# Kernel tuning notes

Measured on AMD Instinct MI355X. Metric: run time of the kernel, lower is better.

Reference implementation:

```python
import jax, jax.numpy as jnp
import numpy as np

D = 768
EXPAND = 4
D_INNER = EXPAND * D
G = 32
EPS = 1e-5


def setup_inputs() -> dict:
    key = jax.random.key(0)
    ks = jax.random.split(key, 10)
    B, T = 16, G * G
    s = lambda fan_in: 1.0 / np.sqrt(fan_in)
    return {
        "x": jax.random.normal(ks[0], (B, T, D), dtype=jnp.float32),
        "norm_w": jnp.ones((D,), dtype=jnp.float32),
        "w_proj": jax.random.normal(ks[1], (D_INNER, D), dtype=jnp.float32) * s(D),
        "w_gate": jax.random.normal(ks[2], (D_INNER, D), dtype=jnp.float32) * s(D),
        "conv_w": jax.random.normal(ks[3], (D_INNER, 1, 3, 3), dtype=jnp.float32) * s(9),
        "conv_b": jax.random.normal(ks[4], (D_INNER,), dtype=jnp.float32) * 0.01,
        "w_out": jax.random.normal(ks[5], (D, D_INNER), dtype=jnp.float32) * s(D_INNER),
        "w_k": jax.random.normal(ks[6], (D, D), dtype=jnp.float32) * s(D),
        "w_v": jax.random.normal(ks[7], (D, D), dtype=jnp.float32) * s(D),
        "log_alpha": jnp.array(0.0, dtype=jnp.float32),  # log(memory_alpha=1.0)
    }


def _rmsnorm(x, w):
    ms = jnp.mean(jnp.square(x.astype(jnp.float32)), axis=-1, keepdims=True)
    return x * jax.lax.rsqrt(ms + EPS).astype(x.dtype) * w


def reference(x, norm_w, w_proj, w_gate, conv_w, conv_b, w_out, w_k, w_v, log_alpha):
    B, T, _ = x.shape
    h = _rmsnorm(x, norm_w)                                   # [B,T,D]
    val = jnp.einsum("btd,ed->bte", h, w_proj)                # [B,T,dI]
    val = val.transpose(0, 2, 1).reshape(B, D_INNER, G, G)    # [B,dI,G,G]
    val = jax.lax.conv_general_dilated(
        val, conv_w, window_strides=(1, 1), padding=((1, 1), (1, 1)),
        dimension_numbers=("NCHW", "OIHW", "NCHW"),
        feature_group_count=D_INNER,
    ) + conv_b[None, :, None, None]
    val = jax.nn.silu(val)
    val = val.reshape(B, D_INNER, T).transpose(0, 2, 1)       # [B,T,dI]
    gated = val * jax.nn.silu(jnp.einsum("btd,ed->bte", h, w_gate))
    out = jnp.einsum("bte,de->btd", gated, w_out)             # [B,T,D]
    K = jnp.einsum("btd,ed->bte", h, w_k)                     # [B,T,D]
    V = jnp.einsum("btd,ed->bte", out, w_v)                   # [B,T,D]
    W = jnp.einsum("btd,bte->bde", K, V) / T                  # [B,D,D]
    read = jnp.einsum("btd,bde->bte", K, W)                   # [B,T,D]
    out = out + jnp.exp(log_alpha) * read
    return x + out
```

## Files before the change

kernel.cpp:

```cpp
#include <hip/hip_runtime.h>
#include <hip/hip_bf16.h>
#include <cstdint>
#include <cstddef>

typedef unsigned short u16;
typedef __attribute__((ext_vector_type(8))) __bf16 bf16x8;
typedef __attribute__((ext_vector_type(4))) float f32x4;
typedef __attribute__((ext_vector_type(8))) unsigned short us8;

#define NDM 768
#define NDI 3072
#define NTT 1024
#define NBB 16
#define NM (NBB*NTT)

__device__ __forceinline__ u16 f2bf(float f) {
  unsigned u = __builtin_bit_cast(unsigned, f);
  u += 0x7fffu + ((u >> 16) & 1u);
  return (u16)(u >> 16);
}
__device__ __forceinline__ float bf2f(u16 b) {
  return __builtin_bit_cast(float, ((unsigned)b) << 16);
}
__device__ __forceinline__ float silu_f(float v) {
  return v * (1.0f / (1.0f + __expf(-v)));
}
__device__ __forceinline__ void gload16(const u16* g, u16* l) {
  __builtin_amdgcn_global_load_lds((const __attribute__((address_space(1))) void*)g,
                                   (__attribute__((address_space(3))) void*)l, 16, 0, 0);
}

__global__ __launch_bounds__(256)
void k_f32_to_bf16(const float* __restrict__ in, u16* __restrict__ out, int n4) {
  const int i = blockIdx.x * 256 + threadIdx.x;
  if (i < n4) {
    float4 v = ((const float4*)in)[i];
    ushort4 o;
    o.x = f2bf(v.x); o.y = f2bf(v.y); o.z = f2bf(v.z); o.w = f2bf(v.w);
    ((ushort4*)out)[i] = o;
  }
}

__global__ __launch_bounds__(256)
void k_convw_t(const float* __restrict__ cw, u16* __restrict__ wTb) {
  const int e = blockIdx.x * 256 + threadIdx.x;
  if (e < NDI) {
#pragma unroll
    for (int t = 0; t < 9; t++) wTb[t * NDI + e] = f2bf(cw[e * 9 + t]);
  }
}

__global__ __launch_bounds__(256)
void k_rmsnorm(const float* __restrict__ x, const float* __restrict__ w, u16* __restrict__ h) {
  const int row  = blockIdx.x * 4 + (threadIdx.x >> 6);
  const int lane = threadIdx.x & 63;
  const float4* xr = (const float4*)(x + (size_t)row * NDM);
  float4 a = xr[lane], b = xr[lane + 64], c = xr[lane + 128];
  float ss = a.x*a.x + a.y*a.y + a.z*a.z + a.w*a.w
           + b.x*b.x + b.y*b.y + b.z*b.z + b.w*b.w
           + c.x*c.x + c.y*c.y + c.z*c.z + c.w*c.w;
#pragma unroll
  for (int off = 32; off > 0; off >>= 1) ss += __shfl_xor(ss, off);
  const float r = rsqrtf(ss * (1.0f / NDM) + 1e-5f);
  const float4* wr = (const float4*)w;
  float4 wa = wr[lane], wb = wr[lane + 64], wc = wr[lane + 128];
  ushort4 oa, ob, oc;
  oa.x = f2bf(a.x * r * wa.x); oa.y = f2bf(a.y * r * wa.y);
  oa.z = f2bf(a.z * r * wa.z); oa.w = f2bf(a.w * r * wa.w);
  ob.x = f2bf(b.x * r * wb.x); ob.y = f2bf(b.y * r * wb.y);
  ob.z = f2bf(b.z * r * wb.z); ob.w = f2bf(b.w * r * wb.w);
  oc.x = f2bf(c.x * r * wc.x); oc.y = f2bf(c.y * r * wc.y);
  oc.z = f2bf(c.z * r * wc.z); oc.w = f2bf(c.w * r * wc.w);
  ushort4* hr = (ushort4*)(h + (size_t)row * NDM);
  hr[lane] = oa; hr[lane + 64] = ob; hr[lane + 128] = oc;
}

__device__ __forceinline__ void stage8k(const u16* Asrc, const u16* Bsrc, u16* smem,
                                        int cur, int wid, int Kd) {
  u16* Ad = smem + cur * 16384 + wid * 512;
  u16* Bd = smem + 32768 + cur * 16384 + wid * 512;
  const size_t blk = (size_t)64 * Kd;
#pragma unroll
  for (int i = 0; i < 4; i++) {
    gload16(Asrc + i * blk, Ad + i * 4096);
    gload16(Bsrc + i * blk, Bd + i * 4096);
  }
}

template <int MODE>
__global__ __launch_bounds__(512, 2)
void k_g8(const u16* __restrict__ A, const u16* __restrict__ B,
          void* __restrict__ C0, void* __restrict__ C1,
          const float* __restrict__ X, const float* __restrict__ scalep,
          int N, int Kd, int nkt, int nTiles,
          long sAb, long sBb, long sCb, int mPerBatchB, long sBm) {
  __shared__ u16 smem[65536];
  const int bz = blockIdx.z;
  A += (size_t)bz * sAb;
  B += (size_t)bz * sBb;
  const int nwg = gridDim.x;
  const int id = blockIdx.x;
  const int sid = ((nwg & 7) == 0) ? ((id & 7) * (nwg >> 3) + (id >> 3)) : id;
  const int mt = sid / nTiles, ntile = sid - mt * nTiles;
  const int m0 = mt * 256, n0 = ntile * 256;
  if (mPerBatchB > 0) B += (size_t)(m0 / mPerBatchB) * sBm;

  const int tid = threadIdx.x;
  const int lane = tid & 63, wid = tid >> 6;
  const int wm = wid >> 2, wn = wid & 3;
  const int fr = lane & 15, l4 = lane >> 4;

  const int srow = tid >> 3;
  const int sslot = (tid & 7) ^ (srow & 7);
  const u16* Asrc = A + (size_t)(m0 + srow) * Kd + sslot * 8;
  const u16* Bsrc = B + (size_t)(n0 + srow) * Kd + sslot * 8;

  f32x4 acc[8][4];
#pragma unroll
  for (int m = 0; m < 8; m++)
#pragma unroll
    for (int n = 0; n < 4; n++) acc[m][n] = (f32x4){0.f, 0.f, 0.f, 0.f};

  stage8k(Asrc,      Bsrc,      smem, 0, wid, Kd);
  stage8k(Asrc + 64, Bsrc + 64, smem, 1, wid, Kd);

  int cur = 0;
#pragma unroll 1
  for (int t = 0; t < nkt; t++) {
    if (t == nkt - 1) asm volatile("s_waitcnt vmcnt(0)" ::: "memory");
    else              asm volatile("s_waitcnt vmcnt(8)" ::: "memory");
    __builtin_amdgcn_s_barrier();

    const u16* Abuf = smem + cur * 16384;
    const u16* Bbuf = smem + 32768 + cur * 16384;

    bf16x8 bfrag[4][2];
#pragma unroll
    for (int nf = 0; nf < 4; nf++) {
      const int brow = wn * 64 + nf * 16 + fr;
#pragma unroll
      for (int s = 0; s < 2; s++)
        bfrag[nf][s] = *(const bf16x8*)&Bbuf[brow * 64 + (((s << 2) + l4) ^ (brow & 7)) * 8];
    }
#pragma unroll
    for (int mf = 0; mf < 8; mf++) {
      const int arow = wm * 128 + mf * 16 + fr;
      bf16x8 a0 = *(const bf16x8*)&Abuf[arow * 64 + ((l4)     ^ (arow & 7)) * 8];
      bf16x8 a1 = *(const bf16x8*)&Abuf[arow * 64 + ((4 + l4) ^ (arow & 7)) * 8];
#pragma unroll
      for (int nf = 0; nf < 4; nf++) {
        acc[mf][nf] = __builtin_amdgcn_mfma_f32_16x16x32_bf16(a0, bfrag[nf][0], acc[mf][nf], 0, 0, 0);
        acc[mf][nf] = __builtin_amdgcn_mfma_f32_16x16x32_bf16(a1, bfrag[nf][1], acc[mf][nf], 0, 0, 0);
      }
    }
    asm volatile("s_waitcnt lgkmcnt(0)" ::: "memory");
    __builtin_amdgcn_s_barrier();
    if (t < nkt - 2) stage8k(Asrc + (size_t)(t + 2) * 64, Bsrc + (size_t)(t + 2) * 64,
                             smem, cur, wid, Kd);
    cur ^= 1;
  }

  float sc = 1.0f;
  if (MODE == 2) sc = __expf(scalep[0]) * (1.0f / 1024.0f);
  const size_t cb = (size_t)bz * sCb;
#pragma unroll
  for (int mf = 0; mf < 8; mf++) {
#pragma unroll
    for (int nf = 0; nf < 4; nf++) {
      const int lc = wn * 64 + nf * 16 + fr;
      const int rb = m0 + wm * 128 + mf * 16 + (l4 << 2);
#pragma unroll
      for (int q = 0; q < 4; q++) {
        float v = acc[mf][nf][q];
        if (MODE == 0) {
          ((u16*)C0)[cb + (size_t)(rb + q) * N + n0 + lc] = f2bf(v);
        } else if (MODE == 2) {
          ((u16*)C0)[cb + (size_t)(rb + q) * N + n0 + lc] = f2bf(v * sc);
        } else if (MODE == 3) {
          const size_t idx = (size_t)(rb + q) * N + n0 + lc;
          ((float*)C0)[idx] = X[idx] + bf2f(((const u16*)C1)[idx]) + v;
        } else {
          const int gc = n0 + lc;
          if (gc < 3072) ((u16*)C0)[(size_t)(rb + q) * 3072 + gc] = f2bf(v);
          else           ((u16*)C1)[(size_t)(rb + q) * 3072 + gc - 3072] = f2bf(silu_f(v));
        }
      }
    }
  }
}

__global__ __launch_bounds__(384)
void k_conv_gate(const u16* __restrict__ val, u16* __restrict__ gate,
                 const u16* __restrict__ wTb, const float* __restrict__ bias) {
  const int tid = threadIdx.x;
  const int m = blockIdx.x * 2 + (tid >= 192);
  const int e0 = (tid % 192) * 16;
  const int j = m & 31, i = (m >> 5) & 31;
  float acc[16];
  {
    const float4* bp = (const float4*)(bias + e0);
    float4 b0 = bp[0], b1 = bp[1], b2 = bp[2], b3 = bp[3];
    acc[0]=b0.x; acc[1]=b0.y; acc[2]=b0.z; acc[3]=b0.w;
    acc[4]=b1.x; acc[5]=b1.y; acc[6]=b1.z; acc[7]=b1.w;
    acc[8]=b2.x; acc[9]=b2.y; acc[10]=b2.z; acc[11]=b2.w;
    acc[12]=b3.x; acc[13]=b3.y; acc[14]=b3.z; acc[15]=b3.w;
  }
  const u16* vb = val + (size_t)m * NDI + e0;
#pragma unroll
  for (int di = -1; di <= 1; di++) {
    if ((unsigned)(i + di) >= 32u) continue;
#pragma unroll
    for (int dj = -1; dj <= 1; dj++) {
      if ((unsigned)(j + dj) >= 32u) continue;
      const u16* vp = vb + (ptrdiff_t)(di * 32 + dj) * NDI;
      us8 v0 = *(const us8*)vp, v1 = *(const us8*)(vp + 8);
      const u16* wp = wTb + ((di + 1) * 3 + (dj + 1)) * NDI + e0;
      us8 w0 = *(const us8*)wp, w1 = *(const us8*)(wp + 8);
#pragma unroll
      for (int q = 0; q < 8; q++) acc[q]     += bf2f(v0[q]) * bf2f(w0[q]);
#pragma unroll
      for (int q = 0; q < 8; q++) acc[8 + q] += bf2f(v1[q]) * bf2f(w1[q]);
    }
  }
  u16* gp = gate + (size_t)m * NDI + e0;
  us8 g0 = *(const us8*)gp, g1 = *(const us8*)(gp + 8);
  us8 o0, o1;
#pragma unroll
  for (int q = 0; q < 8; q++) o0[q] = f2bf(silu_f(acc[q]) * bf2f(g0[q]));
#pragma unroll
  for (int q = 0; q < 8; q++) o1[q] = f2bf(silu_f(acc[8 + q]) * bf2f(g1[q]));
  *(us8*)gp = o0;
  *(us8*)(gp + 8) = o1;
}

__global__ __launch_bounds__(256)
void k_transpose(const u16* __restrict__ in, u16* __restrict__ out) {
  __shared__ u16 tile[64][65];
  const int d0 = blockIdx.x * 64, t0 = blockIdx.y * 64, b = blockIdx.z;
  const int lx = threadIdx.x & 15, ly = threadIdx.x >> 4;
  const u16* ip = in + ((size_t)b * NTT + t0) * NDM + d0;
#pragma unroll
  for (int p = 0; p < 4; p++) {
    const int r = ly + p * 16;
    ushort4 v = *(const ushort4*)(ip + (size_t)r * NDM + lx * 4);
    tile[r][lx * 4 + 0] = v.x; tile[r][lx * 4 + 1] = v.y;
    tile[r][lx * 4 + 2] = v.z; tile[r][lx * 4 + 3] = v.w;
  }
  __syncthreads();
  u16* op = out + ((size_t)b * NDM + d0) * NTT + t0;
#pragma unroll
  for (int p = 0; p < 4; p++) {
    const int r = ly + p * 16;
    ushort4 v;
    v.x = tile[lx * 4 + 0][r]; v.y = tile[lx * 4 + 1][r];
    v.z = tile[lx * 4 + 2][r]; v.w = tile[lx * 4 + 3][r];
    *(ushort4*)(op + (size_t)r * NTT + lx * 4) = v;
  }
}

extern "C" void kernel_launch(void* const* d_in, const int* in_sizes, int n_in,
                              void* d_out, int out_size, void* d_ws, size_t ws_size,
                              hipStream_t stream) {
  const float* x      = (const float*)d_in[0];
  const float* norm_w = (const float*)d_in[1];
  const float* w_proj = (const float*)d_in[2];
  const float* w_gate = (const float*)d_in[3];
  const float* conv_w = (const float*)d_in[4];
  const float* conv_b = (const float*)d_in[5];
  const float* w_out  = (const float*)d_in[6];
  const float* w_k    = (const float*)d_in[7];
  const float* w_v    = (const float*)d_in[8];
  const float* lalpha = (const float*)d_in[9];

  char* ob = (char*)d_out;
  u16* h    = (u16*)(ob);
  u16* wcat = (u16*)(ob + 25165824);
  u16* wob  = (u16*)(ob + 34603008);
  u16* wkb  = (u16*)(ob + 39321600);
  u16* wvb  = (u16*)(ob + 40501248);
  u16* wTb  = (u16*)(ob + 41680896);

  char* ws = (char*)d_ws;
  u16* valp  = (u16*)(ws);
  u16* gateb = (u16*)(ws + 100663296);
  u16* outb  = (u16*)(ws);
  u16* Kbf   = (u16*)(ws + 25165824);
  u16* Vbf   = (u16*)(ws + 50331648);
  u16* Kt    = (u16*)(ws + 100663296);
  u16* Vt    = (u16*)(ws + 125829120);
  u16* Wt    = (u16*)(ws + 150994944);

  k_f32_to_bf16<<<2304, 256, 0, stream>>>(w_proj, wcat,           589824);
  k_f32_to_bf16<<<2304, 256, 0, stream>>>(w_gate, wcat + 2359296, 589824);
  k_f32_to_bf16<<<2304, 256, 0, stream>>>(w_out,  wob, 589824);
  k_f32_to_bf16<<<576,  256, 0, stream>>>(w_k,    wkb, 147456);
  k_f32_to_bf16<<<576,  256, 0, stream>>>(w_v,    wvb, 147456);
  k_convw_t<<<12, 256, 0, stream>>>(conv_w, wTb);

  k_rmsnorm<<<4096, 256, 0, stream>>>(x, norm_w, h);

  k_g8<5><<<1536, 512, 0, stream>>>(h, wcat, valp, gateb, nullptr, nullptr,
                                    3072, 768, 12, 24, 0, 0, 0, 0, 0);
  k_conv_gate<<<8192, 384, 0, stream>>>(valp, gateb, wTb, conv_b);

  k_g8<0><<<192, 512, 0, stream>>>(gateb, wob, outb, nullptr, nullptr, nullptr,
                                   768, 3072, 48, 3, 0, 0, 0, 0, 0);
  k_g8<0><<<192, 512, 0, stream>>>(h, wkb, Kbf, nullptr, nullptr, nullptr,
                                   768, 768, 12, 3, 0, 0, 0, 0, 0);
  k_g8<0><<<192, 512, 0, stream>>>(outb, wvb, Vbf, nullptr, nullptr, nullptr,
                                   768, 768, 12, 3, 0, 0, 0, 0, 0);
  k_transpose<<<dim3(12, 16, 16), 256, 0, stream>>>(Kbf, Kt);
  k_transpose<<<dim3(12, 16, 16), 256, 0, stream>>>(Vbf, Vt);

  k_g8<2><<<dim3(9, 1, 16), 512, 0, stream>>>(Vt, Kt, Wt, nullptr, nullptr, lalpha,
                                              768, 1024, 16, 3,
                                              (long)NDM * NTT, (long)NDM * NTT,
                                              (long)NDM * NDM, 0, 0);
  k_g8<3><<<192, 512, 0, stream>>>(Kbf, Wt, d_out, outb, x, nullptr,
                                   768, 768, 12, 3, 0, 0, 0,
                                   NTT, (long)NDM * NDM);
}
```

Measured before the change: 701.3 us.

## Switch GEMM mainloop to 4-buffer, 32-wide K stages with deeper prefetch

The bf16 MFMA GEMM now moves through K in 32-element stages across four LDS buffers instead of 64-element stages across two. Loads run three stages ahead, which removes the second barrier per iteration. Each stage reads all fragments before issuing the next prefetch, then runs the MFMAs at raised wave priority. In exchange there are twice as many loop iterations and barriers, and the LDS swizzle becomes a 4-slot XOR pattern that may cause more bank conflicts.

Result: no change. 703.3 us (+0.3%).

```diff
diff --git a/kernel.cpp b/kernel.cpp
--- a/kernel.cpp
+++ b/kernel.cpp
@@ -75,24 +75,12 @@
   hr[lane] = oa; hr[lane + 64] = ob; hr[lane + 128] = oc;
 }
 
-__device__ __forceinline__ void stage8k(const u16* Asrc, const u16* Bsrc, u16* smem,
-                                        int cur, int wid, int Kd) {
-  u16* Ad = smem + cur * 16384 + wid * 512;
-  u16* Bd = smem + 32768 + cur * 16384 + wid * 512;
-  const size_t blk = (size_t)64 * Kd;
-#pragma unroll
-  for (int i = 0; i < 4; i++) {
-    gload16(Asrc + i * blk, Ad + i * 4096);
-    gload16(Bsrc + i * blk, Bd + i * 4096);
-  }
-}
-
 template <int MODE>
 __global__ __launch_bounds__(512, 2)
 void k_g8(const u16* __restrict__ A, const u16* __restrict__ B,
           void* __restrict__ C0, void* __restrict__ C1,
           const float* __restrict__ X, const float* __restrict__ scalep,
-          int N, int Kd, int nkt, int nTiles,
+          int N, int Kd, int nst, int nTiles,
           long sAb, long sBb, long sCb, int mPerBatchB, long sBm) {
   __shared__ u16 smem[65536];
   const int bz = blockIdx.z;
@@ -110,10 +98,21 @@
   const int wm = wid >> 2, wn = wid & 3;
   const int fr = lane & 15, l4 = lane >> 4;
 
-  const int srow = tid >> 3;
-  const int sslot = (tid & 7) ^ (srow & 7);
-  const u16* Asrc = A + (size_t)(m0 + srow) * Kd + sslot * 8;
-  const u16* Bsrc = B + (size_t)(n0 + srow) * Kd + sslot * 8;
+  const int rbase = (wid << 4) + (lane >> 2);
+  const int cslot = (lane & 3) ^ ((lane >> 2) & 3);
+  const u16* Ap = A + (size_t)(m0 + rbase) * Kd + cslot * 8;
+  const u16* Bp = B + (size_t)(n0 + rbase) * Kd + cslot * 8;
+  const size_t strideI = (size_t)128 * Kd;
+  const int ldsW = wid * 512;
+
+#define STAGE_G8(s_) {                                         \
+    const int b3_ = (s_) & 3;                                  \
+    const u16* as_ = Ap + (size_t)(s_) * 32;                   \
+    const u16* bs_ = Bp + (size_t)(s_) * 32;                   \
+    u16* ad_ = smem + b3_ * 8192 + ldsW;                       \
+    u16* bd_ = smem + 32768 + b3_ * 8192 + ldsW;               \
+    gload16(as_, ad_);           gload16(as_ + strideI, ad_ + 4096); \
+    gload16(bs_, bd_);           gload16(bs_ + strideI, bd_ + 4096); }
 
   f32x4 acc[8][4];
 #pragma unroll
@@ -121,44 +120,45 @@
 #pragma unroll
     for (int n = 0; n < 4; n++) acc[m][n] = (f32x4){0.f, 0.f, 0.f, 0.f};
 
-  stage8k(Asrc,      Bsrc,      smem, 0, wid, Kd);
-  stage8k(Asrc + 64, Bsrc + 64, smem, 1, wid, Kd);
-
-  int cur = 0;
+  STAGE_G8(0); STAGE_G8(1); STAGE_G8(2);
+
 #pragma unroll 1
-  for (int t = 0; t < nkt; t++) {
-    if (t == nkt - 1) asm volatile("s_waitcnt vmcnt(0)" ::: "memory");
-    else              asm volatile("s_waitcnt vmcnt(8)" ::: "memory");
+  for (int s = 0; s < nst; s++) {
+    const int left = nst - 1 - s;
+    if (left >= 2)      asm volatile("s_waitcnt vmcnt(8)" ::: "memory");
+    else if (left == 1) asm volatile("s_waitcnt vmcnt(4)" ::: "memory");
+    else                asm volatile("s_waitcnt vmcnt(0)" ::: "memory");
     __builtin_amdgcn_s_barrier();
-
-    const u16* Abuf = smem + cur * 16384;
-    const u16* Bbuf = smem + 32768 + cur * 16384;
-
-    bf16x8 bfrag[4][2];
+    __builtin_amdgcn_sched_barrier(0);
+
+    const int b = s & 3;
+    const u16* Ab = smem + b * 8192;
+    const u16* Bb = smem + 32768 + b * 8192;
+
+    bf16x8 bfr[4];
 #pragma unroll
     for (int nf = 0; nf < 4; nf++) {
       const int brow = wn * 64 + nf * 16 + fr;
-#pragma unroll
-      for (int s = 0; s < 2; s++)
-        bfrag[nf][s] = *(const bf16x8*)&Bbuf[brow * 64 + (((s << 2) + l4) ^ (brow & 7)) * 8];
+      bfr[nf] = *(const bf16x8*)&Bb[brow * 32 + ((l4 ^ (brow & 3)) << 3)];
     }
+    bf16x8 af[8];
 #pragma unroll
     for (int mf = 0; mf < 8; mf++) {
       const int arow = wm * 128 + mf * 16 + fr;
-      bf16x8 a0 = *(const bf16x8*)&Abuf[arow * 64 + ((l4)     ^ (arow & 7)) * 8];
-      bf16x8 a1 = *(const bf16x8*)&Abuf[arow * 64 + ((4 + l4) ^ (arow & 7)) * 8];
-#pragma unroll
-      for (int nf = 0; nf < 4; nf++) {
-        acc[mf][nf] = __builtin_amdgcn_mfma_f32_16x16x32_bf16(a0, bfrag[nf][0], acc[mf][nf], 0, 0, 0);
-        acc[mf][nf] = __builtin_amdgcn_mfma_f32_16x16x32_bf16(a1, bfrag[nf][1], acc[mf][nf], 0, 0, 0);
-      }
+      af[mf] = *(const bf16x8*)&Ab[arow * 32 + ((l4 ^ (arow & 3)) << 3)];
     }
-    asm volatile("s_waitcnt lgkmcnt(0)" ::: "memory");
-    __builtin_amdgcn_s_barrier();
-    if (t < nkt - 2) stage8k(Asrc + (size_t)(t + 2) * 64, Bsrc + (size_t)(t + 2) * 64,
-                             smem, cur, wid, Kd);
-    cur ^= 1;
-  }
+
+    if (s + 3 < nst) STAGE_G8(s + 3);
+
+    __builtin_amdgcn_s_setprio(1);
+#pragma unroll
+    for (int mf = 0; mf < 8; mf++)
+#pragma unroll
+      for (int nf = 0; nf < 4; nf++)
+        acc[mf][nf] = __builtin_amdgcn_mfma_f32_16x16x32_bf16(af[mf], bfr[nf], acc[mf][nf], 0, 0, 0);
+    __builtin_amdgcn_s_setprio(0);
+  }
+#undef STAGE_G8
 
   float sc = 1.0f;
   if (MODE == 2) sc = __expf(scalep[0]) * (1.0f / 1024.0f);
@@ -300,23 +300,23 @@
   k_rmsnorm<<<4096, 256, 0, stream>>>(x, norm_w, h);
 
   k_g8<5><<<1536, 512, 0, stream>>>(h, wcat, valp, gateb, nullptr, nullptr,
-                                    3072, 768, 12, 24, 0, 0, 0, 0, 0);
+                                    3072, 768, 24, 24, 0, 0, 0, 0, 0);
   k_conv_gate<<<8192, 384, 0, stream>>>(valp, gateb, wTb, conv_b);
 
   k_g8<0><<<192, 512, 0, stream>>>(gateb, wob, outb, nullptr, nullptr, nullptr,
-                                   768, 3072, 48, 3, 0, 0, 0, 0, 0);
+                                   768, 3072, 96, 3, 0, 0, 0, 0, 0);
   k_g8<0><<<192, 512, 0, stream>>>(h, wkb, Kbf, nullptr, nullptr, nullptr,
-                                   768, 768, 12, 3, 0, 0, 0, 0, 0);
+                                   768, 768, 24, 3, 0, 0, 0, 0, 0);
   k_g8<0><<<192, 512, 0, stream>>>(outb, wvb, Vbf, nullptr, nullptr, nullptr,
-                                   768, 768, 12, 3, 0, 0, 0, 0, 0);
+                                   768, 768, 24, 3, 0, 0, 0, 0, 0);
   k_transpose<<<dim3(12, 16, 16), 256, 0, stream>>>(Kbf, Kt);
   k_transpose<<<dim3(12, 16, 16), 256, 0, stream>>>(Vbf, Vt);
 
   k_g8<2><<<dim3(9, 1, 16), 512, 0, stream>>>(Vt, Kt, Wt, nullptr, nullptr, lalpha,
-                                              768, 1024, 16, 3,
+                                              768, 1024, 32, 3,
                                               (long)NDM * NTT, (long)NDM * NTT,
                                               (long)NDM * NDM, 0, 0);
   k_g8<3><<<192, 512, 0, stream>>>(Kbf, Wt, d_out, outb, x, nullptr,
-                                   768, 768, 12, 3, 0, 0, 0,
+                                   768, 768, 24, 3, 0, 0, 0,
                                    NTT, (long)NDM * NDM);
 }
```
